# Optimization experiments

Hardware: AMD Instinct MI355X
Metric: run time of the kernel (lower is better)

## Reference

```python
import jax, jax.numpy as jnp
import numpy as np

H = 1024      # hidden_dim
F = 4 * H     # expert FFN dim
E = 16        # num_experts
K = 4         # num_experts_per_token


def setup_inputs() -> dict:
    key = jax.random.key(0)
    ks = jax.random.split(key, 10)
    s = 0.02
    return {
        "x": jax.random.normal(ks[0], (2, 1024, H), dtype=jnp.float32),
        # router: Linear(H,H) -> ReLU -> Linear(H,E)
        "Wr1": jax.random.normal(ks[1], (H, H), dtype=jnp.float32) * s,
        "br1": jnp.zeros((H,), dtype=jnp.float32),
        "Wr2": jax.random.normal(ks[2], (H, E), dtype=jnp.float32) * s,
        "br2": jnp.zeros((E,), dtype=jnp.float32),
        # stacked experts: Linear(H,4H) -> GELU -> Linear(4H,H)
        "W1": jax.random.normal(ks[3], (E, H, F), dtype=jnp.float32) * s,
        "b1": jnp.zeros((E, F), dtype=jnp.float32),
        "W2": jax.random.normal(ks[4], (E, F, H), dtype=jnp.float32) * s,
        "b2": jnp.zeros((E, H), dtype=jnp.float32),
    }


def reference(x, Wr1, br1, Wr2, br2, W1, b1, W2, b2):
    B, S, Hd = x.shape
    xf = x.reshape(-1, Hd)                       # [T, H]
    T = xf.shape[0]
    # router logits
    logits = jnp.maximum(xf @ Wr1 + br1, 0.0) @ Wr2 + br2   # [T, E]
    # top-k routing: softmax over the k selected logits
    topw, topi = jax.lax.top_k(logits, K)                    # [T, K]
    topw = jax.nn.softmax(topw, axis=-1)
    # dense combine weights c[t, e] = sum_k topw[t,k] * 1[topi[t,k]==e]
    c = jnp.zeros((T, E), dtype=xf.dtype)
    c = c.at[jnp.arange(T)[:, None], topi].add(topw)         # [T, E]
    # all-experts dense MLP (exact GELU, matching nn.GELU default)
    h = jax.nn.gelu(jnp.einsum('th,ehf->etf', xf, W1) + b1[:, None, :],
                    approximate=False)                       # [E, T, F]
    y = jnp.einsum('etf,efh->eth', h, W2) + b2[:, None, :]   # [E, T, H]
    out = jnp.einsum('eth,te->th', y, c)                     # [T, H]
    return out.reshape(B, S, Hd)
```

## Files before the change

kernel.cpp:

```cpp
#include <hip/hip_runtime.h>
#include <hip/hip_bf16.h>

#define T_TOK 2048
#define H_DIM 1024
#define F_DIM 4096
#define E_NUM 16
#define K_TOP 4

typedef float    floatx4 __attribute__((ext_vector_type(4)));
typedef _Float16 f16x8   __attribute__((ext_vector_type(8)));
typedef _Float16 f16x4   __attribute__((ext_vector_type(4)));

#define MiB (1024ull * 1024ull)
#define LOGIT_OFF ((size_t)0)
#define OFFS_OFF  (256ull * 1024)
#define TOKS_OFF  (320ull * 1024)
#define WSL_OFF   (384ull * 1024)
#define STK_OFF   (448ull * 1024)
#define TILEE_OFF (512ull * 1024)
#define TILEM_OFF (TILEE_OFF + 512)
#define TILEC_OFF (TILEM_OFF + 512)
#define XH_OFF    (1ull * MiB)
#define HBUF_OFF  (8ull * MiB)
#define YBUF_OFF  (72ull * MiB)
#define W1T_OFF   (104ull * MiB)
#define W2T_OFF   (232ull * MiB)
#define WS_NEED_FAST (360ull * MiB)

__device__ __forceinline__ void gload16(const void* g, void* l) {
  __builtin_amdgcn_global_load_lds(
      (const __attribute__((address_space(1))) unsigned int*)g,
      (__attribute__((address_space(3))) unsigned int*)l, 16, 0, 0);
}

__device__ __forceinline__ float gelu_fast(float v) {
  float z = 0.7978845608028654f * (v + 0.044715f * v * v * v);
  float e = __expf(2.f * z);
  float t = 1.f - 2.f / (e + 1.f);
  return 0.5f * v * (1.f + t);
}

__device__ __forceinline__ void cast_x_body(int blk, const float* __restrict__ x,
                                            _Float16* __restrict__ xh) {
  int i = blk * 256 + threadIdx.x;
  const floatx4* xin = reinterpret_cast<const floatx4*>(x) + (size_t)i * 2;
  floatx4 a = xin[0], b = xin[1];
  f16x8 o;
  o[0] = (_Float16)a[0]; o[1] = (_Float16)a[1]; o[2] = (_Float16)a[2]; o[3] = (_Float16)a[3];
  o[4] = (_Float16)b[0]; o[5] = (_Float16)b[1]; o[6] = (_Float16)b[2]; o[7] = (_Float16)b[3];
  *reinterpret_cast<f16x8*>(xh + (size_t)i * 8) = o;
}

__device__ __forceinline__ void tcast4_body(const float* __restrict__ W,
                                            _Float16* __restrict__ Wt, int K, int N,
                                            int e, int k0, int n0base, char* smem) {
  float (*Tt)[64][69] = (float(*)[64][69])smem;
  const float* We = W + (size_t)e * K * N;
  _Float16* dste = Wt + (size_t)e * N * K;
  int t = threadIdx.x;
  int kk = t >> 4, nn = (t & 15) * 4;
  int nr = t >> 3, kc = t & 7;
  floatx4 r[4];
  {
    const float* src = We + (size_t)(k0 + kk) * N + n0base + nn;
#pragma unroll
    for (int j = 0; j < 4; j++)
      r[j] = *reinterpret_cast<const floatx4*>(src + (size_t)(16 * j) * N);
  }
#pragma unroll
  for (int tt = 0; tt < 4; ++tt) {
    int b = tt & 1;
#pragma unroll
    for (int j = 0; j < 4; j++)
      *reinterpret_cast<floatx4*>(&Tt[b][kk + 16 * j][nn]) = r[j];
    if (tt + 1 < 4) {
      const float* src = We + (size_t)(k0 + kk) * N + n0base + (tt + 1) * 64 + nn;
#pragma unroll
      for (int j = 0; j < 4; j++)
        r[j] = *reinterpret_cast<const floatx4*>(src + (size_t)(16 * j) * N);
    }
    asm volatile("s_waitcnt lgkmcnt(0)" ::: "memory");
    __builtin_amdgcn_s_barrier();
    int n0 = n0base + tt * 64;
#pragma unroll
    for (int half = 0; half < 2; half++) {
      int n = nr + half * 32;
      f16x8 o;
#pragma unroll
      for (int j = 0; j < 8; j++) o[j] = (_Float16)Tt[b][kc * 8 + j][n];
      *reinterpret_cast<f16x8*>(dste + (size_t)(n0 + n) * K + k0 + kc * 8) = o;
    }
  }
}

__device__ __forceinline__ void router_gemm1_body(
    int m0, int n0, const float* __restrict__ x, const float* __restrict__ Wr1,
    const float* __restrict__ br1, float* __restrict__ hrf, char* smem) {
  _Float16 (*Ah)[40] = (_Float16(*)[40])(smem);
  _Float16 (*Al)[40] = (_Float16(*)[40])(smem + 5120);
  _Float16 (*Bh)[40] = (_Float16(*)[40])(smem + 10240);
  _Float16 (*Bl)[40] = (_Float16(*)[40])(smem + 15360);
  int tid = threadIdx.x;
  int arow = tid >> 2, achk = tid & 3;
  const float* Arow = x + (size_t)(m0 + arow) * H_DIM + achk * 8;
  int brow = tid >> 3, bq = tid & 7;

  floatx4 acc[2][2];
#pragma unroll
  for (int i = 0; i < 2; i++)
#pragma unroll
    for (int j = 0; j < 2; j++) acc[i][j] = (floatx4){0.f, 0.f, 0.f, 0.f};

  int wv = tid >> 6, lane = tid & 63;
  int wm = wv >> 1, wn = wv & 1;
  int lrow = lane & 15, lk = (lane >> 4) * 8;

  for (int k0 = 0; k0 < H_DIM; k0 += 32) {
    floatx4 a0 = *reinterpret_cast<const floatx4*>(Arow + k0);
    floatx4 a1 = *reinterpret_cast<const floatx4*>(Arow + k0 + 4);
    f16x8 hv, lv;
#pragma unroll
    for (int j = 0; j < 4; j++) {
      _Float16 hi = (_Float16)a0[j]; hv[j] = hi; lv[j] = (_Float16)(a0[j] - (float)hi);
      _Float16 hi2 = (_Float16)a1[j]; hv[4 + j] = hi2; lv[4 + j] = (_Float16)(a1[j] - (float)hi2);
    }
    *reinterpret_cast<f16x8*>(&Ah[arow][achk * 8]) = hv;
    *reinterpret_cast<f16x8*>(&Al[arow][achk * 8]) = lv;
    const float* wp = Wr1 + (size_t)(k0 + brow) * H_DIM + n0 + bq * 4;
    floatx4 w0 = *reinterpret_cast<const floatx4*>(wp);
    floatx4 w1 = *reinterpret_cast<const floatx4*>(wp + 32);
#pragma unroll
    for (int i = 0; i < 4; i++) {
      _Float16 h0 = (_Float16)w0[i];
      Bh[bq * 4 + i][brow] = h0; Bl[bq * 4 + i][brow] = (_Float16)(w0[i] - (float)h0);
      _Float16 h1 = (_Float16)w1[i];
      Bh[32 + bq * 4 + i][brow] = h1; Bl[32 + bq * 4 + i][brow] = (_Float16)(w1[i] - (float)h1);
    }
    __syncthreads();

    f16x8 ah0 = *reinterpret_cast<const f16x8*>(&Ah[32 * wm + lrow][lk]);
    f16x8 ah1 = *reinterpret_cast<const f16x8*>(&Ah[32 * wm + 16 + lrow][lk]);
    f16x8 al0 = *reinterpret_cast<const f16x8*>(&Al[32 * wm + lrow][lk]);
    f16x8 al1 = *reinterpret_cast<const f16x8*>(&Al[32 * wm + 16 + lrow][lk]);
    f16x8 bh0 = *reinterpret_cast<const f16x8*>(&Bh[32 * wn + lrow][lk]);
    f16x8 bh1 = *reinterpret_cast<const f16x8*>(&Bh[32 * wn + 16 + lrow][lk]);
    f16x8 bl0 = *reinterpret_cast<const f16x8*>(&Bl[32 * wn + lrow][lk]);
    f16x8 bl1 = *reinterpret_cast<const f16x8*>(&Bl[32 * wn + 16 + lrow][lk]);

    acc[0][0] = __builtin_amdgcn_mfma_f32_16x16x32_f16(ah0, bh0, acc[0][0], 0, 0, 0);
    acc[0][0] = __builtin_amdgcn_mfma_f32_16x16x32_f16(ah0, bl0, acc[0][0], 0, 0, 0);
    acc[0][0] = __builtin_amdgcn_mfma_f32_16x16x32_f16(al0, bh0, acc[0][0], 0, 0, 0);
    acc[0][1] = __builtin_amdgcn_mfma_f32_16x16x32_f16(ah0, bh1, acc[0][1], 0, 0, 0);
    acc[0][1] = __builtin_amdgcn_mfma_f32_16x16x32_f16(ah0, bl1, acc[0][1], 0, 0, 0);
    acc[0][1] = __builtin_amdgcn_mfma_f32_16x16x32_f16(al0, bh1, acc[0][1], 0, 0, 0);
    acc[1][0] = __builtin_amdgcn_mfma_f32_16x16x32_f16(ah1, bh0, acc[1][0], 0, 0, 0);
    acc[1][0] = __builtin_amdgcn_mfma_f32_16x16x32_f16(ah1, bl0, acc[1][0], 0, 0, 0);
    acc[1][0] = __builtin_amdgcn_mfma_f32_16x16x32_f16(al1, bh0, acc[1][0], 0, 0, 0);
    acc[1][1] = __builtin_amdgcn_mfma_f32_16x16x32_f16(ah1, bh1, acc[1][1], 0, 0, 0);
    acc[1][1] = __builtin_amdgcn_mfma_f32_16x16x32_f16(ah1, bl1, acc[1][1], 0, 0, 0);
    acc[1][1] = __builtin_amdgcn_mfma_f32_16x16x32_f16(al1, bh1, acc[1][1], 0, 0, 0);
    __syncthreads();
  }

#pragma unroll
  for (int am = 0; am < 2; am++) {
#pragma unroll
    for (int bn = 0; bn < 2; bn++) {
      int col = n0 + 32 * wn + 16 * bn + lrow;
      float bv = br1[col];
#pragma unroll
      for (int r = 0; r < 4; r++) {
        int rowt = 32 * wm + 16 * am + (lane >> 4) * 4 + r;
        float v = acc[am][bn][r] + bv;
        hrf[(size_t)(m0 + rowt) * H_DIM + col] = fmaxf(v, 0.f);
      }
    }
  }
}

#define P1_T2 4096
#define P1_RG 512
#define P1_CX 1024
#define P1_T1 4096
#define P1_TOTAL (P1_T2 + P1_RG + P1_CX + P1_T1)
__global__ __launch_bounds__(256) void fusedA_kernel(
    const float* __restrict__ x, const float* __restrict__ Wr1, const float* __restrict__ br1,
    float* __restrict__ hrf, const float* __restrict__ W1, _Float16* __restrict__ W1t,
    const float* __restrict__ W2, _Float16* __restrict__ W2t, _Float16* __restrict__ xh) {
  __shared__ __align__(16) char smem[35840];
  int bid = blockIdx.x;
  if (bid < P1_T2) {
    int e = bid >> 8, nt4 = (bid >> 6) & 3, kt = bid & 63;
    tcast4_body(W2, W2t, F_DIM, H_DIM, e, kt * 64, nt4 * 256, smem);
  } else if (bid < P1_T2 + P1_RG) {
    int g = bid - P1_T2;
    router_gemm1_body((g >> 4) * 64, (g & 15) * 64, x, Wr1, br1, hrf, smem);
  } else if (bid < P1_T2 + P1_RG + P1_CX) {
    cast_x_body(bid - P1_T2 - P1_RG, x, xh);
  } else {
    int idx = bid - P1_T2 - P1_RG - P1_CX;
    int e = idx >> 8, nt4 = (idx >> 4) & 15, kt = idx & 15;
    tcast4_body(W1, W1t, H_DIM, F_DIM, e, kt * 64, nt4 * 256, smem);
  }
}

__global__ __launch_bounds__(256) void router_logits_kernel(
    const float* __restrict__ hrf, const float* __restrict__ Wr2,
    const float* __restrict__ br2, float* __restrict__ logits) {
  int t = blockIdx.x * 4 + (threadIdx.x >> 6);
  int lane = threadIdx.x & 63;
  float acc[E_NUM];
#pragma unroll
  for (int e = 0; e < E_NUM; e++) acc[e] = 0.f;
  const float* hr = hrf + (size_t)t * H_DIM;
#pragma unroll 4
  for (int i = 0; i < H_DIM / 64; i++) {
    int k = lane + 64 * i;
    float a = hr[k];
    const floatx4* w4 = reinterpret_cast<const floatx4*>(Wr2 + (size_t)k * E_NUM);
    floatx4 w0 = w4[0], w1 = w4[1], w2 = w4[2], w3 = w4[3];
#pragma unroll
    for (int j = 0; j < 4; j++) {
      acc[j]      += a * w0[j];
      acc[4 + j]  += a * w1[j];
      acc[8 + j]  += a * w2[j];
      acc[12 + j] += a * w3[j];
    }
  }
#pragma unroll
  for (int e = 0; e < E_NUM; e++) {
    float v = acc[e];
    for (int off = 32; off > 0; off >>= 1) v += __shfl_xor(v, off);
    if (lane == e) logits[(size_t)t * E_NUM + e] = v + br2[e];
  }
}

__global__ __launch_bounds__(1024) void routing_kernel(
    const float* __restrict__ logits, int* __restrict__ offs,
    int* __restrict__ toks, float* __restrict__ wsl, int* __restrict__ stk,
    int* __restrict__ tileE, int* __restrict__ tileM, int* __restrict__ tileC) {
  __shared__ int cnt[E_NUM], cur[E_NUM], loff[E_NUM + 1];
  int tid = threadIdx.x;
  if (tid < E_NUM) { cnt[tid] = 0; cur[tid] = 0; }
  __syncthreads();
  int ti[2][K_TOP]; float tw[2][K_TOP];
#pragma unroll
  for (int u = 0; u < 2; u++) {
    int t = u * 1024 + tid;
    float lg[E_NUM];
#pragma unroll
    for (int e = 0; e < E_NUM; e++) lg[e] = logits[(size_t)t * E_NUM + e];
    unsigned int used = 0;
    float vals[K_TOP];
#pragma unroll
    for (int k = 0; k < K_TOP; k++) {
      float best = -1e30f; int bi = 0;
#pragma unroll
      for (int e = 0; e < E_NUM; e++) {
        if (!((used >> e) & 1u) && lg[e] > best) { best = lg[e]; bi = e; }
      }
      used |= (1u << bi);
      vals[k] = best; ti[u][k] = bi;
    }
    float m = vals[0], s = 0.f;
#pragma unroll
    for (int k = 0; k < K_TOP; k++) { tw[u][k] = expf(vals[k] - m); s += tw[u][k]; }
    float inv = 1.f / s;
#pragma unroll
    for (int k = 0; k < K_TOP; k++) {
      tw[u][k] *= inv;
      atomicAdd(&cnt[ti[u][k]], 1);
    }
  }
  __syncthreads();
  if (tid == 0) {
    int acc = 0;
    loff[0] = 0; offs[0] = 0;
    for (int e = 0; e < E_NUM; e++) { acc += cnt[e]; loff[e + 1] = acc; offs[e + 1] = acc; }
    int idx = 0;
    for (int e = 0; e < E_NUM; e++) {
      for (int m0 = 0; m0 < cnt[e]; m0 += 128) { tileE[idx] = e; tileM[idx] = m0; idx++; }
    }
    tileC[0] = idx;
  }
  __syncthreads();
#pragma unroll
  for (int u = 0; u < 2; u++) {
    int t = u * 1024 + tid;
#pragma unroll
    for (int k = 0; k < K_TOP; k++) {
      int e = ti[u][k];
      int pos = atomicAdd(&cur[e], 1);
      int slot = loff[e] + pos;
      toks[slot] = t;
      wsl[slot] = tw[u][k];
      stk[t * K_TOP + k] = slot;
    }
  }
}

__global__ void combine_kernel(const _Float16* __restrict__ ybuf, const int* __restrict__ stk,
                               float* __restrict__ out) {
  int i = blockIdx.x * 256 + threadIdx.x;
  size_t p = (size_t)i * 8;
  int t = (int)(p >> 10);
  int h = (int)(p & 1023);
  float s[8] = {0.f, 0.f, 0.f, 0.f, 0.f, 0.f, 0.f, 0.f};
#pragma unroll
  for (int k = 0; k < K_TOP; k++) {
    int slot = stk[t * K_TOP + k];
    f16x8 v = *reinterpret_cast<const f16x8*>(ybuf + (size_t)slot * H_DIM + h);
#pragma unroll
    for (int j = 0; j < 8; j++) s[j] += (float)v[j];
  }
  floatx4 o0 = {s[0], s[1], s[2], s[3]};
  floatx4 o1 = {s[4], s[5], s[6], s[7]};
  *reinterpret_cast<floatx4*>(out + p) = o0;
  *reinterpret_cast<floatx4*>(out + p + 4) = o1;
}

template <int KK, int ACT, bool GATHER, bool SCALE>
__device__ __forceinline__ void moe_gemm_body(
    int ti, int n0, const _Float16* __restrict__ A, const _Float16* __restrict__ Bt,
    const float* __restrict__ bias, _Float16* __restrict__ Out,
    const int* __restrict__ offsets, const int* __restrict__ toklist,
    const float* __restrict__ wslot, const int* __restrict__ tileE,
    const int* __restrict__ tileM, const int* __restrict__ tileC,
    int N, char* smem) {
  if (ti >= tileC[0]) return;
  const int K = KK;
  int e = tileE[ti], m0 = tileM[ti];
  int base = offsets[e], cnt = offsets[e + 1] - base;

  _Float16 (*As)[128][32] = reinterpret_cast<_Float16(*)[128][32]>(smem);
  _Float16 (*Bs)[128][32] = reinterpret_cast<_Float16(*)[128][32]>(smem + 24576);

  int tid = threadIdx.x;
  int w = tid >> 6, lane = tid & 63;
  int wm = w >> 1, wn = w & 1;
  int lrow = lane & 15;

  int ar0 = w * 32 + (lane >> 2);
  int ar1 = ar0 + 16;
  int ach = (((lane & 3) ^ ((lane >> 3) & 3))) * 8;
  int mr0 = m0 + ar0; if (mr0 >= cnt) mr0 = cnt - 1;
  int mr1 = m0 + ar1; if (mr1 >= cnt) mr1 = cnt - 1;
  const _Float16* gA0 = A + (long)(GATHER ? toklist[base + mr0] : (base + mr0)) * K + ach;
  const _Float16* gA1 = A + (long)(GATHER ? toklist[base + mr1] : (base + mr1)) * K + ach;
  const _Float16* bge = Bt + (size_t)e * N * K;
  const _Float16* gB0 = bge + (long)(n0 + ar0) * K + ach;
  const _Float16* gB1 = bge + (long)(n0 + ar1) * K + ach;

  int phys8 = ((lane >> 4) ^ ((lrow >> 1) & 3)) * 8;

#define STAGE3(buf, kk) do { \
    gload16(gA0 + (kk), &As[buf][w * 32][0]); \
    gload16(gA1 + (kk), &As[buf][w * 32 + 16][0]); \
    gload16(gB0 + (kk), &Bs[buf][w * 32][0]); \
    gload16(gB1 + (kk), &Bs[buf][w * 32 + 16][0]); \
  } while (0)

#define COMPUTE3(buf) do { \
    f16x8 a[4], b[4]; \
    _Pragma("unroll") \
    for (int i = 0; i < 4; i++) { \
      a[i] = *reinterpret_cast<const f16x8*>(&As[buf][wm * 64 + i * 16 + lrow][phys8]); \
      b[i] = *reinterpret_cast<const f16x8*>(&Bs[buf][wn * 64 + i * 16 + lrow][phys8]); \
    } \
    __builtin_amdgcn_s_setprio(1); \
    _Pragma("unroll") \
    for (int i = 0; i < 4; i++) \
      _Pragma("unroll") \
      for (int j = 0; j < 4; j++) \
        acc[i][j] = __builtin_amdgcn_mfma_f32_16x16x32_f16(a[i], b[j], acc[i][j], 0, 0, 0); \
    __builtin_amdgcn_s_setprio(0); \
  } while (0)

  floatx4 acc[4][4];
#pragma unroll
  for (int i = 0; i < 4; i++)
#pragma unroll
    for (int j = 0; j < 4; j++) acc[i][j] = (floatx4){0.f, 0.f, 0.f, 0.f};

  constexpr int nk = KK / 32;
  STAGE3(0, 0);
  STAGE3(1, 32);

#pragma unroll 3
  for (int it = 0; it < nk - 1; ++it) {
    asm volatile("s_waitcnt vmcnt(4)" ::: "memory");
    __builtin_amdgcn_s_barrier();
    if (it + 2 < nk) STAGE3((it + 2) % 3, (it + 2) * 32);
    COMPUTE3(it % 3);
  }
  asm volatile("s_waitcnt vmcnt(0)" ::: "memory");
  __builtin_amdgcn_s_barrier();
  COMPUTE3((nk - 1) % 3);

#undef STAGE3
#undef COMPUTE3

  const float* be = bias + (size_t)e * N;
#pragma unroll
  for (int fm = 0; fm < 4; fm++) {
#pragma unroll
    for (int fn = 0; fn < 4; fn++) {
      int col = n0 + wn * 64 + fn * 16 + lrow;
      float bv = be[col];
#pragma unroll
      for (int r = 0; r < 4; r++) {
        int rowt = wm * 64 + fm * 16 + (lane >> 4) * 4 + r;
        int mg = m0 + rowt;
        if (mg < cnt) {
          float v = acc[fm][fn][r] + bv;
          if (ACT == 2) v = gelu_fast(v);
          long orow = base + mg;
          if (SCALE) v *= wslot[orow];
          Out[orow * (long)N + col] = (_Float16)v;
        }
      }
    }
  }
}

__global__ __launch_bounds__(256) void moe_gemm1_kernel(
    const _Float16* __restrict__ xh, const _Float16* __restrict__ W1t,
    const float* __restrict__ b1, _Float16* __restrict__ hbuf,
    const int* __restrict__ offsets, const int* __restrict__ toklist,
    const int* __restrict__ tileE, const int* __restrict__ tileM, const int* __restrict__ tileC) {
  __shared__ __align__(16) char smem[49152];
  int x = blockIdx.x;
  int ti = (x & 7) * 10 + (x >> 3);
  moe_gemm_body<H_DIM, 2, true, false>(ti, blockIdx.y * 128, xh, W1t, b1, hbuf,
                                       offsets, toklist, nullptr, tileE, tileM, tileC,
                                       F_DIM, smem);
}

__global__ __launch_bounds__(256) void moe_gemm2_kernel(
    const _Float16* __restrict__ hbuf, const _Float16* __restrict__ W2t,
    const float* __restrict__ b2, _Float16* __restrict__ ybuf,
    const int* __restrict__ offsets, const float* __restrict__ wslot,
    const int* __restrict__ tileE, const int* __restrict__ tileM, const int* __restrict__ tileC) {
  __shared__ __align__(16) char smem[49152];
  int x = blockIdx.x;
  int ti = (x & 7) * 10 + (x >> 3);
  moe_gemm_body<F_DIM, 0, false, true>(ti, blockIdx.y * 128, hbuf, W2t, b2, ybuf,
                                       offsets, nullptr, wslot, tileE, tileM, tileC,
                                       H_DIM, smem);
}

template <int ACT, bool GATHER, bool OFFS, bool SCALE>
__global__ __launch_bounds__(256) void moe_gemm(
    const _Float16* __restrict__ A, const float* __restrict__ W,
    const float* __restrict__ bias, _Float16* __restrict__ Out,
    const int* __restrict__ offsets, const int* __restrict__ toklist,
    const float* __restrict__ wslot, int M, int N, int K) {
  int e = blockIdx.z;
  int base = 0, cnt = M;
  if (OFFS) { base = offsets[e]; cnt = offsets[e + 1] - base; }
  int m0 = blockIdx.y * 64;
  if (m0 >= cnt) return;
  int n0 = blockIdx.x * 64;
  const float* We = W + (size_t)e * K * N;
  const float* be = bias + (size_t)e * N;

  __shared__ _Float16 As[64][40];
  __shared__ _Float16 Bs[64][40];

  int tid = threadIdx.x;
  int arow = tid >> 2, achk = tid & 3;
  int am_idx = m0 + arow; if (am_idx > cnt - 1) am_idx = cnt - 1;
  long arowg = GATHER ? (long)toklist[base + am_idx] : (long)(base + am_idx);
  const _Float16* Arow = A + arowg * (long)K + achk * 8;

  int brow = tid >> 3, bq = tid & 7;

  floatx4 acc[2][2];
#pragma unroll
  for (int i = 0; i < 2; i++)
#pragma unroll
    for (int j = 0; j < 2; j++) acc[i][j] = (floatx4){0.f, 0.f, 0.f, 0.f};

  int wv = tid >> 6, lane = tid & 63;
  int wm = wv >> 1, wn = wv & 1;
  int lrow = lane & 15, lk = (lane >> 4) * 8;

  for (int k0 = 0; k0 < K; k0 += 32) {
    *reinterpret_cast<f16x8*>(&As[arow][achk * 8]) = *reinterpret_cast<const f16x8*>(Arow + k0);
    const float* wp = We + (size_t)(k0 + brow) * N + n0 + bq * 4;
    floatx4 w0 = *reinterpret_cast<const floatx4*>(wp);
    floatx4 w1 = *reinterpret_cast<const floatx4*>(wp + 32);
#pragma unroll
    for (int i = 0; i < 4; i++) {
      Bs[bq * 4 + i][brow]      = (_Float16)w0[i];
      Bs[32 + bq * 4 + i][brow] = (_Float16)w1[i];
    }
    __syncthreads();

    f16x8 a0 = *reinterpret_cast<const f16x8*>(&As[32 * wm + lrow][lk]);
    f16x8 a1 = *reinterpret_cast<const f16x8*>(&As[32 * wm + 16 + lrow][lk]);
    f16x8 b0 = *reinterpret_cast<const f16x8*>(&Bs[32 * wn + lrow][lk]);
    f16x8 b1 = *reinterpret_cast<const f16x8*>(&Bs[32 * wn + 16 + lrow][lk]);
    acc[0][0] = __builtin_amdgcn_mfma_f32_16x16x32_f16(a0, b0, acc[0][0], 0, 0, 0);
    acc[0][1] = __builtin_amdgcn_mfma_f32_16x16x32_f16(a0, b1, acc[0][1], 0, 0, 0);
    acc[1][0] = __builtin_amdgcn_mfma_f32_16x16x32_f16(a1, b0, acc[1][0], 0, 0, 0);
    acc[1][1] = __builtin_amdgcn_mfma_f32_16x16x32_f16(a1, b1, acc[1][1], 0, 0, 0);
    __syncthreads();
  }

#pragma unroll
  for (int am = 0; am < 2; am++) {
#pragma unroll
    for (int bn = 0; bn < 2; bn++) {
      int col = n0 + 32 * wn + 16 * bn + lrow;
      float bv = be[col];
#pragma unroll
      for (int r = 0; r < 4; r++) {
        int rowt = 32 * wm + 16 * am + (lane >> 4) * 4 + r;
        int mg = m0 + rowt;
        if (mg < cnt) {
          float v = acc[am][bn][r] + bv;
          if (ACT == 2) v = gelu_fast(v);
          long orow = base + mg;
          if (SCALE) v *= wslot[orow];
          Out[orow * (long)N + col] = (_Float16)v;
        }
      }
    }
  }
}

__global__ void cast_x_kernel(const float* __restrict__ x, _Float16* __restrict__ xh) {
  cast_x_body(blockIdx.x, x, xh);
}

__global__ __launch_bounds__(256) void router_gemm1_kernel(
    const float* __restrict__ x, const float* __restrict__ Wr1,
    const float* __restrict__ br1, float* __restrict__ hrf) {
  __shared__ __align__(16) char smem[20480];
  router_gemm1_body(blockIdx.y * 64, blockIdx.x * 64, x, Wr1, br1, hrf, smem);
}

extern "C" void kernel_launch(void* const* d_in, const int* in_sizes, int n_in,
                              void* d_out, int out_size, void* d_ws, size_t ws_size,
                              hipStream_t stream) {
  const float* x   = (const float*)d_in[0];
  const float* Wr1 = (const float*)d_in[1];
  const float* br1 = (const float*)d_in[2];
  const float* Wr2 = (const float*)d_in[3];
  const float* br2 = (const float*)d_in[4];
  const float* W1  = (const float*)d_in[5];
  const float* b1  = (const float*)d_in[6];
  const float* W2  = (const float*)d_in[7];
  const float* b2  = (const float*)d_in[8];
  float* out = (float*)d_out;

  char* ws = (char*)d_ws;
  float* logits = (float*)(ws + LOGIT_OFF);
  int*   offs   = (int*)(ws + OFFS_OFF);
  int*   toks   = (int*)(ws + TOKS_OFF);
  float* wsl    = (float*)(ws + WSL_OFF);
  int*   stk    = (int*)(ws + STK_OFF);
  int*   tileE  = (int*)(ws + TILEE_OFF);
  int*   tileM  = (int*)(ws + TILEM_OFF);
  int*   tileC  = (int*)(ws + TILEC_OFF);
  _Float16* xh   = (_Float16*)(ws + XH_OFF);
  float*    hrf  = (float*)(ws + HBUF_OFF);
  _Float16* hbuf = (_Float16*)(ws + HBUF_OFF);
  _Float16* ybuf = (_Float16*)(ws + YBUF_OFF);
  _Float16* W1t  = (_Float16*)(ws + W1T_OFF);
  _Float16* W2t  = (_Float16*)(ws + W2T_OFF);

  bool fast = ws_size >= WS_NEED_FAST;

  if (fast) {
    fusedA_kernel<<<P1_TOTAL, 256, 0, stream>>>(x, Wr1, br1, hrf, W1, W1t, W2, W2t, xh);
  } else {
    cast_x_kernel<<<(T_TOK * H_DIM / 8) / 256, 256, 0, stream>>>(x, xh);
    router_gemm1_kernel<<<dim3(H_DIM / 64, T_TOK / 64), 256, 0, stream>>>(x, Wr1, br1, hrf);
  }

  router_logits_kernel<<<T_TOK / 4, 256, 0, stream>>>(hrf, Wr2, br2, logits);
  routing_kernel<<<1, 1024, 0, stream>>>(logits, offs, toks, wsl, stk, tileE, tileM, tileC);

  if (fast) {
    moe_gemm1_kernel<<<dim3(80, F_DIM / 128), 256, 0, stream>>>(xh, W1t, b1, hbuf, offs, toks,
                                                                tileE, tileM, tileC);
    moe_gemm2_kernel<<<dim3(80, H_DIM / 128), 256, 0, stream>>>(hbuf, W2t, b2, ybuf, offs, wsl,
                                                                tileE, tileM, tileC);
  } else {
    moe_gemm<2, true, true, false><<<dim3(F_DIM / 64, T_TOK / 64, E_NUM), 256, 0, stream>>>(
        xh, W1, b1, hbuf, offs, toks, nullptr, T_TOK, F_DIM, H_DIM);
    moe_gemm<0, false, true, true><<<dim3(H_DIM / 64, T_TOK / 64, E_NUM), 256, 0, stream>>>(
        hbuf, W2, b2, ybuf, offs, nullptr, wsl, T_TOK, H_DIM, F_DIM);
  }

  combine_kernel<<<(T_TOK * H_DIM / 8) / 256, 256, 0, stream>>>(ybuf, stk, out);
}
```

Measured before the change: 490.3 us.

## Pre-tile transposed expert weights into contiguous swizzled 128x32 blocks

The weight transpose-cast now writes W1/W2 in fp16 as contiguous 128x32 tiles, with the LDS swizzle applied ahead of time. Each B-tile load in the expert GEMM becomes one fully contiguous 8KB read instead of 128 strided rows. The transpose kernel is restructured around a smaller shared buffer with a 128-column layout. This aims to improve memory coalescing and TLB behaviour for the B loads, at the cost of a more complex transpose with possible LDS bank conflicts.

```diff
diff --git a/kernel.cpp b/kernel.cpp
--- a/kernel.cpp
+++ b/kernel.cpp
@@ -9,7 +9,6 @@
 
 typedef float    floatx4 __attribute__((ext_vector_type(4)));
 typedef _Float16 f16x8   __attribute__((ext_vector_type(8)));
-typedef _Float16 f16x4   __attribute__((ext_vector_type(4)));
 
 #define MiB (1024ull * 1024ull)
 #define LOGIT_OFF ((size_t)0)
@@ -51,44 +50,49 @@
   *reinterpret_cast<f16x8*>(xh + (size_t)i * 8) = o;
 }
 
-__device__ __forceinline__ void tcast4_body(const float* __restrict__ W,
-                                            _Float16* __restrict__ Wt, int K, int N,
-                                            int e, int k0, int n0base, char* smem) {
-  float (*Tt)[64][69] = (float(*)[64][69])smem;
+__device__ __forceinline__ void tcast_tile_body(const float* __restrict__ W,
+                                                _Float16* __restrict__ Wtiles, int K, int N,
+                                                int e, int kg, int ns, char* smem) {
+  float (*Tt)[129] = (float(*)[129])smem;
   const float* We = W + (size_t)e * K * N;
-  _Float16* dste = Wt + (size_t)e * N * K;
+  int n0 = ns * 128;
   int t = threadIdx.x;
-  int kk = t >> 4, nn = (t & 15) * 4;
-  int nr = t >> 3, kc = t & 7;
-  floatx4 r[4];
+  int lr = t >> 3, lc = (t & 7) * 16;
+  int wr = t >> 1, hp = t & 1;
+  _Float16* tbase = Wtiles +
+      (((size_t)e * (size_t)(N >> 7) + (size_t)ns) * (size_t)(K >> 5) + (size_t)kg * 4) * 4096;
+
+  floatx4 rr[4];
   {
-    const float* src = We + (size_t)(k0 + kk) * N + n0base + nn;
-#pragma unroll
-    for (int j = 0; j < 4; j++)
-      r[j] = *reinterpret_cast<const floatx4*>(src + (size_t)(16 * j) * N);
-  }
-#pragma unroll
-  for (int tt = 0; tt < 4; ++tt) {
-    int b = tt & 1;
-#pragma unroll
-    for (int j = 0; j < 4; j++)
-      *reinterpret_cast<floatx4*>(&Tt[b][kk + 16 * j][nn]) = r[j];
-    if (tt + 1 < 4) {
-      const float* src = We + (size_t)(k0 + kk) * N + n0base + (tt + 1) * 64 + nn;
-#pragma unroll
-      for (int j = 0; j < 4; j++)
-        r[j] = *reinterpret_cast<const floatx4*>(src + (size_t)(16 * j) * N);
+    const float* s = We + (size_t)(kg * 128 + lr) * N + n0 + lc;
+#pragma unroll
+    for (int q = 0; q < 4; q++) rr[q] = *reinterpret_cast<const floatx4*>(s + q * 4);
+  }
+#pragma unroll
+  for (int it = 0; it < 4; ++it) {
+    if (it > 0) {
+      asm volatile("s_waitcnt lgkmcnt(0)" ::: "memory");
+      __builtin_amdgcn_s_barrier();
+    }
+#pragma unroll
+    for (int q = 0; q < 4; q++)
+      *reinterpret_cast<floatx4*>(&Tt[lr][lc + q * 4]) = rr[q];
+    if (it + 1 < 4) {
+      const float* s = We + (size_t)(kg * 128 + (it + 1) * 32 + lr) * N + n0 + lc;
+#pragma unroll
+      for (int q = 0; q < 4; q++) rr[q] = *reinterpret_cast<const floatx4*>(s + q * 4);
     }
     asm volatile("s_waitcnt lgkmcnt(0)" ::: "memory");
     __builtin_amdgcn_s_barrier();
-    int n0 = n0base + tt * 64;
-#pragma unroll
-    for (int half = 0; half < 2; half++) {
-      int n = nr + half * 32;
+    _Float16* tp = tbase + (size_t)it * 4096 + (size_t)wr * 32 + hp * 16;
+#pragma unroll
+    for (int pp = 0; pp < 2; pp++) {
+      int p = 2 * hp + pp;
+      int c = p ^ ((wr >> 1) & 3);
       f16x8 o;
 #pragma unroll
-      for (int j = 0; j < 8; j++) o[j] = (_Float16)Tt[b][kc * 8 + j][n];
-      *reinterpret_cast<f16x8*>(dste + (size_t)(n0 + n) * K + k0 + kc * 8) = o;
+      for (int j = 0; j < 8; j++) o[j] = (_Float16)Tt[8 * c + j][wr];
+      *reinterpret_cast<f16x8*>(tp + pp * 8) = o;
     }
   }
 }
@@ -187,11 +191,12 @@
     const float* __restrict__ x, const float* __restrict__ Wr1, const float* __restrict__ br1,
     float* __restrict__ hrf, const float* __restrict__ W1, _Float16* __restrict__ W1t,
     const float* __restrict__ W2, _Float16* __restrict__ W2t, _Float16* __restrict__ xh) {
-  __shared__ __align__(16) char smem[35840];
+  __shared__ __align__(16) char smem[20480];
   int bid = blockIdx.x;
   if (bid < P1_T2) {
-    int e = bid >> 8, nt4 = (bid >> 6) & 3, kt = bid & 63;
-    tcast4_body(W2, W2t, F_DIM, H_DIM, e, kt * 64, nt4 * 256, smem);
+    int e = bid >> 8, rem = bid & 255;
+    int ns = rem >> 5, kg = rem & 31;
+    tcast_tile_body(W2, W2t, F_DIM, H_DIM, e, kg, ns, smem);
   } else if (bid < P1_T2 + P1_RG) {
     int g = bid - P1_T2;
     router_gemm1_body((g >> 4) * 64, (g & 15) * 64, x, Wr1, br1, hrf, smem);
@@ -199,8 +204,9 @@
     cast_x_body(bid - P1_T2 - P1_RG, x, xh);
   } else {
     int idx = bid - P1_T2 - P1_RG - P1_CX;
-    int e = idx >> 8, nt4 = (idx >> 4) & 15, kt = idx & 15;
-    tcast4_body(W1, W1t, H_DIM, F_DIM, e, kt * 64, nt4 * 256, smem);
+    int e = idx >> 8, rem = idx & 255;
+    int ns = rem >> 3, kg = rem & 7;
+    tcast_tile_body(W1, W1t, H_DIM, F_DIM, e, kg, ns, smem);
   }
 }
 
@@ -347,17 +353,17 @@
   int mr1 = m0 + ar1; if (mr1 >= cnt) mr1 = cnt - 1;
   const _Float16* gA0 = A + (long)(GATHER ? toklist[base + mr0] : (base + mr0)) * K + ach;
   const _Float16* gA1 = A + (long)(GATHER ? toklist[base + mr1] : (base + mr1)) * K + ach;
-  const _Float16* bge = Bt + (size_t)e * N * K;
-  const _Float16* gB0 = bge + (long)(n0 + ar0) * K + ach;
-  const _Float16* gB1 = bge + (long)(n0 + ar1) * K + ach;
+  const _Float16* gB = Bt +
+      (((size_t)e * (size_t)(N >> 7) + (size_t)(n0 >> 7)) * (size_t)(KK >> 5)) * 4096 +
+      (size_t)w * 1024 + (size_t)lane * 8;
 
   int phys8 = ((lane >> 4) ^ ((lrow >> 1) & 3)) * 8;
 
 #define STAGE3(buf, kk) do { \
     gload16(gA0 + (kk), &As[buf][w * 32][0]); \
     gload16(gA1 + (kk), &As[buf][w * 32 + 16][0]); \
-    gload16(gB0 + (kk), &Bs[buf][w * 32][0]); \
-    gload16(gB1 + (kk), &Bs[buf][w * 32 + 16][0]); \
+    gload16(gB + (size_t)(kk) * 128, &Bs[buf][w * 32][0]); \
+    gload16(gB + (size_t)(kk) * 128 + 512, &Bs[buf][w * 32 + 16][0]); \
   } while (0)
 
 #define COMPUTE3(buf) do { \
```

New measurement: 497.7 us. No clear change (+1.5%).
